# Kernel tuning notes

Measured on AMD Instinct MI355X. Metric: run time of the kernel, lower is better.

Reference implementation:

```python
import jax, jax.numpy as jnp
import numpy as np

HIDDEN = 1024
FFN = 4096
N_EXPERTS = 8
TOP_K = 2


def setup_inputs() -> dict:
    key = jax.random.key(0)
    ks = jax.random.split(key, 6)
    x = jax.random.normal(ks[0], (2, 2048, HIDDEN), dtype=jnp.float32)
    Wr = jax.random.normal(ks[1], (N_EXPERTS, HIDDEN), dtype=jnp.float32) * 0.02
    W1 = jax.random.normal(ks[2], (N_EXPERTS, FFN, HIDDEN), dtype=jnp.float32) * 0.02
    b1 = jnp.zeros((N_EXPERTS, FFN), dtype=jnp.float32)
    W2 = jax.random.normal(ks[3], (N_EXPERTS, HIDDEN, FFN), dtype=jnp.float32) * 0.02
    b2 = jnp.zeros((N_EXPERTS, HIDDEN), dtype=jnp.float32)
    return {"x": x, "Wr": Wr, "W1": W1, "b1": b1, "W2": W2, "b2": b2}


def reference(x, Wr, W1, b1, W2, b2):
    # x: [B, S, D]; Wr: [E, D]; W1: [E, F, D]; W2: [E, D, F]
    B, S, D = x.shape
    E = Wr.shape[0]
    xf = x.reshape(-1, D)                              # [T, D]
    T = xf.shape[0]
    logits = xf @ Wr.T                                 # [T, E]
    probs = jax.nn.softmax(logits, axis=-1)
    top_v, top_i = jax.lax.top_k(probs, TOP_K)         # [T, K]
    top_v = top_v / jnp.sum(top_v, axis=-1, keepdims=True)
    # combine weights: zero except the top-k experts per token
    comb = jnp.zeros((T, E), dtype=xf.dtype).at[jnp.arange(T)[:, None], top_i].add(top_v)
    # run every expert densely (same math as gather/FFN/weighted-scatter)
    h = jax.nn.gelu(jnp.einsum('td,efd->etf', xf, W1) + b1[:, None, :], approximate=False)  # [E, T, F]
    y = jnp.einsum('etf,edf->etd', h, W2) + b2[:, None, :]                                   # [E, T, D]
    out = jnp.einsum('etd,te->td', y, comb)            # weighted combine
    return out.reshape(B, S, D)
```

## Files before the change

kernel.cpp:

```cpp
#include <hip/hip_runtime.h>

#define HIDDEN 1024
#define FFN    4096
#define NEXP   8
#define TOKENS 4096
#define ASSIGN 8192

typedef __attribute__((ext_vector_type(8))) short s8v;
typedef __attribute__((ext_vector_type(4))) float f4v;

__device__ __forceinline__ float bf2f(ushort u) {
    return __uint_as_float(((unsigned int)u) << 16);
}
__device__ __forceinline__ ushort f2bf(float f) {
    unsigned int x = __float_as_uint(f);
    return (ushort)((x + 0x7fffu + ((x >> 16) & 1u)) >> 16);
}

#define GLDS16(g, l) __builtin_amdgcn_global_load_lds( \
    (const __attribute__((address_space(1))) unsigned int*)(g), \
    (__attribute__((address_space(3))) unsigned int*)(l), 16, 0, 0)

__global__ void conv_kernel(const float4* __restrict__ src, ushort4* __restrict__ dst) {
    const int i = blockIdx.x * blockDim.x + threadIdx.x;
    const float4 v = src[i];
    ushort4 o;
    o.x = f2bf(v.x); o.y = f2bf(v.y); o.z = f2bf(v.z); o.w = f2bf(v.w);
    dst[i] = o;
}

__global__ void router_kernel(const float* __restrict__ x, const float* __restrict__ Wr,
                              int* __restrict__ counts, int* __restrict__ topk_idx,
                              float* __restrict__ topk_w) {
    const int tok  = blockIdx.x;
    const int lane = threadIdx.x;
    float acc[NEXP];
#pragma unroll
    for (int e = 0; e < NEXP; ++e) acc[e] = 0.f;
#pragma unroll
    for (int i = 0; i < HIDDEN / 64; ++i) {
        const int idx = i * 64 + lane;
        const float xv = x[(size_t)tok * HIDDEN + idx];
#pragma unroll
        for (int e = 0; e < NEXP; ++e) acc[e] += xv * Wr[e * HIDDEN + idx];
    }
#pragma unroll
    for (int e = 0; e < NEXP; ++e) {
#pragma unroll
        for (int off = 32; off > 0; off >>= 1) acc[e] += __shfl_xor(acc[e], off);
    }
    if (lane == 0) {
        int i0 = 0;
        for (int e = 1; e < NEXP; ++e) if (acc[e] > acc[i0]) i0 = e;
        int i1 = (i0 == 0) ? 1 : 0;
        for (int e = 0; e < NEXP; ++e) if (e != i0 && acc[e] > acc[i1]) i1 = e;
        const float e1 = expf(acc[i1] - acc[i0]);
        const float s  = 1.f + e1;
        topk_idx[tok * 2 + 0] = i0;
        topk_idx[tok * 2 + 1] = i1;
        topk_w[tok * 2 + 0]   = 1.f / s;
        topk_w[tok * 2 + 1]   = e1 / s;
        atomicAdd(&counts[i0], 1);
        atomicAdd(&counts[i1], 1);
    }
}

__global__ void prefix_kernel(const int* __restrict__ counts, int* __restrict__ offsets,
                              int* __restrict__ cursors) {
    if (threadIdx.x == 0) {
        int s = 0;
        for (int e = 0; e < NEXP; ++e) { offsets[e] = s; cursors[e] = s; s += counts[e]; }
        offsets[NEXP] = s;
    }
}

__global__ void scatter_kernel(const int* __restrict__ topk_idx, const float* __restrict__ topk_w,
                               int* __restrict__ cursors, int* __restrict__ token_list,
                               float* __restrict__ weight_list, int* __restrict__ slot_of) {
    const int a = blockIdx.x * blockDim.x + threadIdx.x;
    if (a >= ASSIGN) return;
    const int e   = topk_idx[a];
    const int pos = atomicAdd(&cursors[e], 1);
    token_list[pos]  = a >> 1;
    weight_list[pos] = topk_w[a];
    slot_of[a]       = pos;
}

__global__ __launch_bounds__(256)
void gemm1_kernel(const ushort* __restrict__ x, const ushort* __restrict__ W1,
                  const float* __restrict__ b1, const int* __restrict__ token_list,
                  const int* __restrict__ counts, const int* __restrict__ offsets,
                  ushort* __restrict__ h) {
    const int e      = blockIdx.z;
    const int n_e    = counts[e];
    const int tile_m = blockIdx.y;
    if (n_e <= 0 || tile_m * 128 >= n_e) return;
    const int tile_n = blockIdx.x;
    const int base   = offsets[e];

    __shared__ __align__(16) ushort As[128 * 32];
    __shared__ __align__(16) ushort Bs[128 * 32];

    const int t    = threadIdx.x;
    const int lane = t & 63;
    const int wv   = t >> 6;
    const int srow = t >> 2;
    const int scol = (t & 3) * 8;

    const int r0 = tile_m * 128 + srow;
    const int r1 = r0 + 64;
    const int tokA0 = token_list[base + (r0 < n_e ? r0 : n_e - 1)];
    const int tokA1 = token_list[base + (r1 < n_e ? r1 : n_e - 1)];
    const ushort* gA0 = x + (size_t)tokA0 * HIDDEN + scol;
    const ushort* gA1 = x + (size_t)tokA1 * HIDDEN + scol;
    const ushort* gB0 = W1 + ((size_t)e * FFN + tile_n * 128 + srow) * HIDDEN + scol;
    const ushort* gB1 = W1 + ((size_t)e * FFN + tile_n * 128 + 64 + srow) * HIDDEN + scol;

    ushort* lA0 = As + wv * 512;
    ushort* lA1 = As + 2048 + wv * 512;
    ushort* lB0 = Bs + wv * 512;
    ushort* lB1 = Bs + 2048 + wv * 512;

    f4v acc[4][4];
#pragma unroll
    for (int i = 0; i < 4; ++i)
#pragma unroll
        for (int j = 0; j < 4; ++j) { f4v z = {0.f, 0.f, 0.f, 0.f}; acc[i][j] = z; }

    const int row_off = (wv & 1) * 64;
    const int col_off = (wv >> 1) * 64;
    const int l15 = lane & 15;
    const int lq  = lane >> 4;

    for (int k0 = 0; k0 < HIDDEN; k0 += 32) {
        GLDS16(gA0 + k0, lA0);
        GLDS16(gA1 + k0, lA1);
        GLDS16(gB0 + k0, lB0);
        GLDS16(gB1 + k0, lB1);
        __syncthreads();
        s8v a[4], b[4];
#pragma unroll
        for (int i = 0; i < 4; ++i) a[i] = *(const s8v*)(As + (row_off + i * 16 + l15) * 32 + lq * 8);
#pragma unroll
        for (int j = 0; j < 4; ++j) b[j] = *(const s8v*)(Bs + (col_off + j * 16 + l15) * 32 + lq * 8);
#pragma unroll
        for (int i = 0; i < 4; ++i)
#pragma unroll
            for (int j = 0; j < 4; ++j)
                acc[i][j] = __builtin_amdgcn_mfma_f32_16x16x32_bf16(a[i], b[j], acc[i][j], 0, 0, 0);
        __syncthreads();
    }

    const int mrem = n_e - tile_m * 128;
#pragma unroll
    for (int i = 0; i < 4; ++i) {
#pragma unroll
        for (int r = 0; r < 4; ++r) {
            const int m_loc = row_off + i * 16 + lq * 4 + r;
            if (m_loc < mrem) {
                const size_t hrow = (size_t)(base + tile_m * 128 + m_loc) * FFN;
#pragma unroll
                for (int j = 0; j < 4; ++j) {
                    const int colF = tile_n * 128 + col_off + j * 16 + l15;
                    float v = acc[i][j][r] + b1[e * FFN + colF];
                    v = 0.5f * v * (1.0f + erff(v * 0.70710678118654752f));
                    h[hrow + colF] = f2bf(v);
                }
            }
        }
    }
}

__global__ __launch_bounds__(256)
void gemm2_kernel(const ushort* __restrict__ h, const ushort* __restrict__ W2,
                  const float* __restrict__ b2, const float* __restrict__ weight_list,
                  const int* __restrict__ counts, const int* __restrict__ offsets,
                  ushort* __restrict__ y) {
    const int e      = blockIdx.z;
    const int n_e    = counts[e];
    const int tile_m = blockIdx.y;
    if (n_e <= 0 || tile_m * 128 >= n_e) return;
    const int tile_n = blockIdx.x;
    const int base   = offsets[e];

    __shared__ __align__(16) ushort As[128 * 32];
    __shared__ __align__(16) ushort Bs[128 * 32];

    const int t    = threadIdx.x;
    const int lane = t & 63;
    const int wv   = t >> 6;
    const int srow = t >> 2;
    const int scol = (t & 3) * 8;

    const int r0 = tile_m * 128 + srow;
    const int r1 = r0 + 64;
    const int slot0 = base + (r0 < n_e ? r0 : n_e - 1);
    const int slot1 = base + (r1 < n_e ? r1 : n_e - 1);
    const ushort* gA0 = h + (size_t)slot0 * FFN + scol;
    const ushort* gA1 = h + (size_t)slot1 * FFN + scol;
    const ushort* gB0 = W2 + ((size_t)e * HIDDEN + tile_n * 128 + srow) * FFN + scol;
    const ushort* gB1 = W2 + ((size_t)e * HIDDEN + tile_n * 128 + 64 + srow) * FFN + scol;

    ushort* lA0 = As + wv * 512;
    ushort* lA1 = As + 2048 + wv * 512;
    ushort* lB0 = Bs + wv * 512;
    ushort* lB1 = Bs + 2048 + wv * 512;

    f4v acc[4][4];
#pragma unroll
    for (int i = 0; i < 4; ++i)
#pragma unroll
        for (int j = 0; j < 4; ++j) { f4v z = {0.f, 0.f, 0.f, 0.f}; acc[i][j] = z; }

    const int row_off = (wv & 1) * 64;
    const int col_off = (wv >> 1) * 64;
    const int l15 = lane & 15;
    const int lq  = lane >> 4;

    for (int k0 = 0; k0 < FFN; k0 += 32) {
        GLDS16(gA0 + k0, lA0);
        GLDS16(gA1 + k0, lA1);
        GLDS16(gB0 + k0, lB0);
        GLDS16(gB1 + k0, lB1);
        __syncthreads();
        s8v a[4], b[4];
#pragma unroll
        for (int i = 0; i < 4; ++i) a[i] = *(const s8v*)(As + (row_off + i * 16 + l15) * 32 + lq * 8);
#pragma unroll
        for (int j = 0; j < 4; ++j) b[j] = *(const s8v*)(Bs + (col_off + j * 16 + l15) * 32 + lq * 8);
#pragma unroll
        for (int i = 0; i < 4; ++i)
#pragma unroll
            for (int j = 0; j < 4; ++j)
                acc[i][j] = __builtin_amdgcn_mfma_f32_16x16x32_bf16(a[i], b[j], acc[i][j], 0, 0, 0);
        __syncthreads();
    }

    const int mrem = n_e - tile_m * 128;
#pragma unroll
    for (int i = 0; i < 4; ++i) {
#pragma unroll
        for (int r = 0; r < 4; ++r) {
            const int m_loc = row_off + i * 16 + lq * 4 + r;
            if (m_loc < mrem) {
                const int slot = base + tile_m * 128 + m_loc;
                const float wgt = weight_list[slot];
#pragma unroll
                for (int j = 0; j < 4; ++j) {
                    const int colD = tile_n * 128 + col_off + j * 16 + l15;
                    const float v = acc[i][j][r] + b2[e * HIDDEN + colD];
                    y[(size_t)slot * HIDDEN + colD] = f2bf(v * wgt);
                }
            }
        }
    }
}

__global__ void combine_kernel(const int* __restrict__ slot_of, const ushort* __restrict__ y,
                               float* __restrict__ out) {
    const int idx = blockIdx.x * blockDim.x + threadIdx.x;
    const int t = idx >> 8;
    const int d = (idx & 255) * 4;
    const int s0 = slot_of[t * 2 + 0];
    const int s1 = slot_of[t * 2 + 1];
    const ushort4 a = *(const ushort4*)(y + (size_t)s0 * HIDDEN + d);
    const ushort4 b = *(const ushort4*)(y + (size_t)s1 * HIDDEN + d);
    float4 o;
    o.x = bf2f(a.x) + bf2f(b.x);
    o.y = bf2f(a.y) + bf2f(b.y);
    o.z = bf2f(a.z) + bf2f(b.z);
    o.w = bf2f(a.w) + bf2f(b.w);
    *(float4*)(out + (size_t)t * HIDDEN + d) = o;
}

extern "C" void kernel_launch(void* const* d_in, const int* in_sizes, int n_in,
                              void* d_out, int out_size, void* d_ws, size_t ws_size,
                              hipStream_t stream) {
    const float* x  = (const float*)d_in[0];
    const float* Wr = (const float*)d_in[1];
    const float* W1 = (const float*)d_in[2];
    const float* b1 = (const float*)d_in[3];
    const float* W2 = (const float*)d_in[4];
    const float* b2 = (const float*)d_in[5];
    float* out = (float*)d_out;

    char* ws = (char*)d_ws;
    int*    counts      = (int*)(ws + 0);
    int*    offsets     = (int*)(ws + 256);
    int*    cursors     = (int*)(ws + 512);
    int*    topk_idx    = (int*)(ws + 1024);
    float*  topk_w      = (float*)(ws + 1024 + 32768);
    int*    slot_of     = (int*)(ws + 1024 + 65536);
    int*    token_list  = (int*)(ws + 1024 + 98304);
    float*  weight_list = (float*)(ws + 1024 + 131072);
    ushort* x_bf        = (ushort*)(ws + (1 << 20));
    ushort* wbuf        = (ushort*)(ws + (1 << 20) + 8388608);
    ushort* h           = (ushort*)(ws + (1 << 20) + 8388608 + 67108864);
    ushort* y           = (ushort*)(ws + (1 << 20) + 8388608 + 2 * 67108864ull);

    const int NW = NEXP * FFN * HIDDEN;

    hipMemsetAsync(counts, 0, 64, stream);
    conv_kernel<<<(TOKENS * HIDDEN / 4) / 256, 256, 0, stream>>>((const float4*)x, (ushort4*)x_bf);
    conv_kernel<<<(NW / 4) / 256, 256, 0, stream>>>((const float4*)W1, (ushort4*)wbuf);

    router_kernel<<<TOKENS, 64, 0, stream>>>(x, Wr, counts, topk_idx, topk_w);
    prefix_kernel<<<1, 64, 0, stream>>>(counts, offsets, cursors);
    scatter_kernel<<<ASSIGN / 256, 256, 0, stream>>>(topk_idx, topk_w, cursors,
                                                     token_list, weight_list, slot_of);

    gemm1_kernel<<<dim3(FFN / 128, ASSIGN / 128, NEXP), 256, 0, stream>>>(
        x_bf, wbuf, b1, token_list, counts, offsets, h);

    conv_kernel<<<(NW / 4) / 256, 256, 0, stream>>>((const float4*)W2, (ushort4*)wbuf);

    gemm2_kernel<<<dim3(HIDDEN / 128, ASSIGN / 128, NEXP), 256, 0, stream>>>(
        h, wbuf, b2, weight_list, counts, offsets, y);

    combine_kernel<<<(TOKENS * HIDDEN / 4) / 256, 256, 0, stream>>>(slot_of, y, out);
}
```

Before: 694.3 us.

## Replace LDS-staged GEMM tiles with register double-buffered direct global loads

Both expert GEMM kernels drop shared-memory staging and block barriers. Each wave loads its MFMA fragments straight from global memory into registers, with a two-stage register double buffer. This removes syncthreads and LDS round trips but duplicates global loads across waves, since A and B rows are no longer shared via LDS. The fp32-to-bf16 conversion kernel also now handles eight elements per thread with 16-byte stores.

```diff
diff --git a/kernel.cpp b/kernel.cpp
--- a/kernel.cpp
+++ b/kernel.cpp
@@ -6,8 +6,9 @@
 #define TOKENS 4096
 #define ASSIGN 8192
 
-typedef __attribute__((ext_vector_type(8))) short s8v;
-typedef __attribute__((ext_vector_type(4))) float f4v;
+typedef __attribute__((ext_vector_type(8))) short  s8v;
+typedef __attribute__((ext_vector_type(4))) float  f4v;
+typedef __attribute__((ext_vector_type(8))) ushort u8v;
 
 __device__ __forceinline__ float bf2f(ushort u) {
     return __uint_as_float(((unsigned int)u) << 16);
@@ -17,15 +18,14 @@
     return (ushort)((x + 0x7fffu + ((x >> 16) & 1u)) >> 16);
 }
 
-#define GLDS16(g, l) __builtin_amdgcn_global_load_lds( \
-    (const __attribute__((address_space(1))) unsigned int*)(g), \
-    (__attribute__((address_space(3))) unsigned int*)(l), 16, 0, 0)
-
-__global__ void conv_kernel(const float4* __restrict__ src, ushort4* __restrict__ dst) {
+__global__ void conv_kernel(const float4* __restrict__ src, u8v* __restrict__ dst, int n8) {
     const int i = blockIdx.x * blockDim.x + threadIdx.x;
-    const float4 v = src[i];
-    ushort4 o;
-    o.x = f2bf(v.x); o.y = f2bf(v.y); o.z = f2bf(v.z); o.w = f2bf(v.w);
+    if (i >= n8) return;
+    const float4 v0 = src[i * 2];
+    const float4 v1 = src[i * 2 + 1];
+    u8v o;
+    o[0] = f2bf(v0.x); o[1] = f2bf(v0.y); o[2] = f2bf(v0.z); o[3] = f2bf(v0.w);
+    o[4] = f2bf(v1.x); o[5] = f2bf(v1.y); o[6] = f2bf(v1.z); o[7] = f2bf(v1.w);
     dst[i] = o;
 }
 
@@ -86,6 +86,25 @@
     slot_of[a]       = pos;
 }
 
+#define LOADAB(A_, B_, k0_)                                   \
+    do {                                                      \
+        _Pragma("unroll")                                     \
+        for (int i_ = 0; i_ < 4; ++i_) {                      \
+            A_[i_] = *(const s8v*)(pa[i_] + (k0_));           \
+            B_[i_] = *(const s8v*)(pb[i_] + (k0_));           \
+        }                                                     \
+    } while (0)
+
+#define MFMA16(A_, B_)                                                            \
+    do {                                                                          \
+        _Pragma("unroll")                                                         \
+        for (int i_ = 0; i_ < 4; ++i_)                                            \
+            _Pragma("unroll")                                                     \
+            for (int j_ = 0; j_ < 4; ++j_)                                        \
+                acc[i_][j_] = __builtin_amdgcn_mfma_f32_16x16x32_bf16(            \
+                    A_[i_], B_[j_], acc[i_][j_], 0, 0, 0);                        \
+    } while (0)
+
 __global__ __launch_bounds__(256)
 void gemm1_kernel(const ushort* __restrict__ x, const ushort* __restrict__ W1,
                   const float* __restrict__ b1, const int* __restrict__ token_list,
@@ -98,58 +117,46 @@
     const int tile_n = blockIdx.x;
     const int base   = offsets[e];
 
-    __shared__ __align__(16) ushort As[128 * 32];
-    __shared__ __align__(16) ushort Bs[128 * 32];
-
-    const int t    = threadIdx.x;
-    const int lane = t & 63;
-    const int wv   = t >> 6;
-    const int srow = t >> 2;
-    const int scol = (t & 3) * 8;
-
-    const int r0 = tile_m * 128 + srow;
-    const int r1 = r0 + 64;
-    const int tokA0 = token_list[base + (r0 < n_e ? r0 : n_e - 1)];
-    const int tokA1 = token_list[base + (r1 < n_e ? r1 : n_e - 1)];
-    const ushort* gA0 = x + (size_t)tokA0 * HIDDEN + scol;
-    const ushort* gA1 = x + (size_t)tokA1 * HIDDEN + scol;
-    const ushort* gB0 = W1 + ((size_t)e * FFN + tile_n * 128 + srow) * HIDDEN + scol;
-    const ushort* gB1 = W1 + ((size_t)e * FFN + tile_n * 128 + 64 + srow) * HIDDEN + scol;
-
-    ushort* lA0 = As + wv * 512;
-    ushort* lA1 = As + 2048 + wv * 512;
-    ushort* lB0 = Bs + wv * 512;
-    ushort* lB1 = Bs + 2048 + wv * 512;
-
-    f4v acc[4][4];
-#pragma unroll
-    for (int i = 0; i < 4; ++i)
-#pragma unroll
-        for (int j = 0; j < 4; ++j) { f4v z = {0.f, 0.f, 0.f, 0.f}; acc[i][j] = z; }
-
+    const int lane = threadIdx.x & 63;
+    const int wv   = threadIdx.x >> 6;
     const int row_off = (wv & 1) * 64;
     const int col_off = (wv >> 1) * 64;
     const int l15 = lane & 15;
     const int lq  = lane >> 4;
 
-    for (int k0 = 0; k0 < HIDDEN; k0 += 32) {
-        GLDS16(gA0 + k0, lA0);
-        GLDS16(gA1 + k0, lA1);
-        GLDS16(gB0 + k0, lB0);
-        GLDS16(gB1 + k0, lB1);
-        __syncthreads();
-        s8v a[4], b[4];
-#pragma unroll
-        for (int i = 0; i < 4; ++i) a[i] = *(const s8v*)(As + (row_off + i * 16 + l15) * 32 + lq * 8);
-#pragma unroll
-        for (int j = 0; j < 4; ++j) b[j] = *(const s8v*)(Bs + (col_off + j * 16 + l15) * 32 + lq * 8);
-#pragma unroll
-        for (int i = 0; i < 4; ++i)
-#pragma unroll
-            for (int j = 0; j < 4; ++j)
-                acc[i][j] = __builtin_amdgcn_mfma_f32_16x16x32_bf16(a[i], b[j], acc[i][j], 0, 0, 0);
-        __syncthreads();
-    }
+    const ushort* pa[4];
+    const ushort* pb[4];
+#pragma unroll
+    for (int i = 0; i < 4; ++i) {
+        int r = tile_m * 128 + row_off + i * 16 + l15;
+        r = r < n_e ? r : n_e - 1;
+        const int tok = token_list[base + r];
+        pa[i] = x + (size_t)tok * HIDDEN + lq * 8;
+    }
+#pragma unroll
+    for (int j = 0; j < 4; ++j) {
+        const int c = tile_n * 128 + col_off + j * 16 + l15;
+        pb[j] = W1 + ((size_t)e * FFN + c) * HIDDEN + lq * 8;
+    }
+
+    f4v acc[4][4];
+#pragma unroll
+    for (int i = 0; i < 4; ++i)
+#pragma unroll
+        for (int j = 0; j < 4; ++j) { f4v z = {0.f, 0.f, 0.f, 0.f}; acc[i][j] = z; }
+
+    s8v A0[4], B0[4], A1[4], B1[4];
+    LOADAB(A0, B0, 0);
+    int k0 = 0;
+    for (; k0 + 64 < HIDDEN; k0 += 64) {
+        LOADAB(A1, B1, k0 + 32);
+        MFMA16(A0, B0);
+        LOADAB(A0, B0, k0 + 64);
+        MFMA16(A1, B1);
+    }
+    LOADAB(A1, B1, k0 + 32);
+    MFMA16(A0, B0);
+    MFMA16(A1, B1);
 
     const int mrem = n_e - tile_m * 128;
 #pragma unroll
@@ -183,58 +190,45 @@
     const int tile_n = blockIdx.x;
     const int base   = offsets[e];
 
-    __shared__ __align__(16) ushort As[128 * 32];
-    __shared__ __align__(16) ushort Bs[128 * 32];
-
-    const int t    = threadIdx.x;
-    const int lane = t & 63;
-    const int wv   = t >> 6;
-    const int srow = t >> 2;
-    const int scol = (t & 3) * 8;
-
-    const int r0 = tile_m * 128 + srow;
-    const int r1 = r0 + 64;
-    const int slot0 = base + (r0 < n_e ? r0 : n_e - 1);
-    const int slot1 = base + (r1 < n_e ? r1 : n_e - 1);
-    const ushort* gA0 = h + (size_t)slot0 * FFN + scol;
-    const ushort* gA1 = h + (size_t)slot1 * FFN + scol;
-    const ushort* gB0 = W2 + ((size_t)e * HIDDEN + tile_n * 128 + srow) * FFN + scol;
-    const ushort* gB1 = W2 + ((size_t)e * HIDDEN + tile_n * 128 + 64 + srow) * FFN + scol;
-
-    ushort* lA0 = As + wv * 512;
-    ushort* lA1 = As + 2048 + wv * 512;
-    ushort* lB0 = Bs + wv * 512;
-    ushort* lB1 = Bs + 2048 + wv * 512;
-
-    f4v acc[4][4];
-#pragma unroll
-    for (int i = 0; i < 4; ++i)
-#pragma unroll
-        for (int j = 0; j < 4; ++j) { f4v z = {0.f, 0.f, 0.f, 0.f}; acc[i][j] = z; }
-
+    const int lane = threadIdx.x & 63;
+    const int wv   = threadIdx.x >> 6;
     const int row_off = (wv & 1) * 64;
     const int col_off = (wv >> 1) * 64;
     const int l15 = lane & 15;
     const int lq  = lane >> 4;
 
-    for (int k0 = 0; k0 < FFN; k0 += 32) {
-        GLDS16(gA0 + k0, lA0);
-        GLDS16(gA1 + k0, lA1);
-        GLDS16(gB0 + k0, lB0);
-        GLDS16(gB1 + k0, lB1);
-        __syncthreads();
-        s8v a[4], b[4];
-#pragma unroll
-        for (int i = 0; i < 4; ++i) a[i] = *(const s8v*)(As + (row_off + i * 16 + l15) * 32 + lq * 8);
-#pragma unroll
-        for (int j = 0; j < 4; ++j) b[j] = *(const s8v*)(Bs + (col_off + j * 16 + l15) * 32 + lq * 8);
-#pragma unroll
-        for (int i = 0; i < 4; ++i)
-#pragma unroll
-            for (int j = 0; j < 4; ++j)
-                acc[i][j] = __builtin_amdgcn_mfma_f32_16x16x32_bf16(a[i], b[j], acc[i][j], 0, 0, 0);
-        __syncthreads();
-    }
+    const ushort* pa[4];
+    const ushort* pb[4];
+#pragma unroll
+    for (int i = 0; i < 4; ++i) {
+        int r = tile_m * 128 + row_off + i * 16 + l15;
+        r = r < n_e ? r : n_e - 1;
+        pa[i] = h + (size_t)(base + r) * FFN + lq * 8;
+    }
+#pragma unroll
+    for (int j = 0; j < 4; ++j) {
+        const int c = tile_n * 128 + col_off + j * 16 + l15;
+        pb[j] = W2 + ((size_t)e * HIDDEN + c) * FFN + lq * 8;
+    }
+
+    f4v acc[4][4];
+#pragma unroll
+    for (int i = 0; i < 4; ++i)
+#pragma unroll
+        for (int j = 0; j < 4; ++j) { f4v z = {0.f, 0.f, 0.f, 0.f}; acc[i][j] = z; }
+
+    s8v A0[4], B0[4], A1[4], B1[4];
+    LOADAB(A0, B0, 0);
+    int k0 = 0;
+    for (; k0 + 64 < FFN; k0 += 64) {
+        LOADAB(A1, B1, k0 + 32);
+        MFMA16(A0, B0);
+        LOADAB(A0, B0, k0 + 64);
+        MFMA16(A1, B1);
+    }
+    LOADAB(A1, B1, k0 + 32);
+    MFMA16(A0, B0);
+    MFMA16(A1, B1);
 
     const int mrem = n_e - tile_m * 128;
 #pragma unroll
@@ -301,8 +295,10 @@
     const int NW = NEXP * FFN * HIDDEN;
 
     hipMemsetAsync(counts, 0, 64, stream);
-    conv_kernel<<<(TOKENS * HIDDEN / 4) / 256, 256, 0, stream>>>((const float4*)x, (ushort4*)x_bf);
-    conv_kernel<<<(NW / 4) / 256, 256, 0, stream>>>((const float4*)W1, (ushort4*)wbuf);
+    conv_kernel<<<(TOKENS * HIDDEN / 8 + 255) / 256, 256, 0, stream>>>(
+        (const float4*)x, (u8v*)x_bf, TOKENS * HIDDEN / 8);
+    conv_kernel<<<(NW / 8 + 255) / 256, 256, 0, stream>>>(
+        (const float4*)W1, (u8v*)wbuf, NW / 8);
 
     router_kernel<<<TOKENS, 64, 0, stream>>>(x, Wr, counts, topk_idx, topk_w);
     prefix_kernel<<<1, 64, 0, stream>>>(counts, offsets, cursors);
@@ -312,7 +308,8 @@
     gemm1_kernel<<<dim3(FFN / 128, ASSIGN / 128, NEXP), 256, 0, stream>>>(
         x_bf, wbuf, b1, token_list, counts, offsets, h);
 
-    conv_kernel<<<(NW / 4) / 256, 256, 0, stream>>>((const float4*)W2, (ushort4*)wbuf);
+    conv_kernel<<<(NW / 8 + 255) / 256, 256, 0, stream>>>(
+        (const float4*)W2, (u8v*)wbuf, NW / 8);
 
     gemm2_kernel<<<dim3(HIDDEN / 128, ASSIGN / 128, NEXP), 256, 0, stream>>>(
         h, wbuf, b2, weight_list, counts, offsets, y);
```

Measured after the change: 1.188 ms. 1.71x slower.
